# Kernel tuning notes

Measured on AMD Instinct MI355X. Metric: run time of the kernel, lower is better.

The kernel has to match this reference:

```python
import jax, jax.numpy as jnp
import numpy as np

B, N_IN, D, K, N = 8, 256, 128, 1024, 4096
EMA_GAMMA = 0.99


def setup_inputs() -> dict:
    key = jax.random.key(0)
    k1, k2, k3 = jax.random.split(key, 3)
    z = jax.random.normal(k1, (B, N_IN, N), dtype=jnp.float32)
    # Conv1d(n_in, d, 1, bias=False) == a (d, n_in) matmul; xavier-ish scale
    W_lin = jax.random.normal(k2, (D, N_IN), dtype=jnp.float32) * (1.0 / np.sqrt(N_IN))
    # codebook initialized xavier_uniform with gain=10 in the original
    lim = 10.0 * np.sqrt(6.0 / (K + D))
    emb = jax.random.uniform(k3, (K, D), dtype=jnp.float32, minval=-lim, maxval=lim)
    ema_numer = emb * (1.0 - EMA_GAMMA)
    ema_denom = jnp.ones((K,), dtype=jnp.float32) * (1.0 - EMA_GAMMA)
    return {"z": z, "W_lin": W_lin, "emb": emb,
            "ema_numer": ema_numer, "ema_denom": ema_denom}


def reference(z, W_lin, emb, ema_numer, ema_denom):
    # ze: (B, d, N) -- 1x1 conv == channel matmul
    ze = jnp.einsum('bcn,dc->bdn', z, W_lin)
    sg_emb = jax.lax.stop_gradient(emb)           # codebook is stop-gradded

    # scaled L2 distance:  ||ze - q|| / (||ze|| + ||q||), shape (B, K, N)
    ze_sq = jnp.sum(ze * ze, axis=1)              # (B, N)
    q_sq = jnp.sum(sg_emb * sg_emb, axis=1)       # (K,)
    dots = jnp.einsum('bdn,kd->bkn', ze, sg_emb)  # (B, K, N)
    dist_sq = jnp.maximum(ze_sq[:, None, :] + q_sq[None, :, None] - 2.0 * dots, 0.0)
    den = jnp.sqrt(ze_sq)[:, None, :] + jnp.sqrt(q_sq)[None, :, None]
    snorm = jnp.sqrt(dist_sq) / den               # (B, K, N)

    min_ind = jnp.argmin(snorm, axis=1)           # (B, N) int
    zq = jnp.moveaxis(sg_emb[min_ind], -1, 1)     # (B, d, N)

    # ReplaceGrad: forward value = zq, gradient routed to ze (straight-through)
    zq_rg = ze + jax.lax.stop_gradient(zq - ze)

    # EMA codebook statistics (scatter-add over codebook indices)
    flat_ind = min_ind.reshape(-1)                             # (B*N,)
    ze_flat = jax.lax.stop_gradient(
        jnp.moveaxis(ze, 1, 2).reshape(-1, ze.shape[1]))       # (B*N, d)
    z_sum = jax.ops.segment_sum(ze_flat, flat_ind, num_segments=K)   # (K, d)
    n_sum = jax.ops.segment_sum(jnp.ones(flat_ind.shape, ze.dtype),
                                flat_ind, num_segments=K)            # (K,)
    ema_numer_new = EMA_GAMMA * ema_numer + (1.0 - EMA_GAMMA) * z_sum
    ema_denom_new = EMA_GAMMA * ema_denom + (1.0 - EMA_GAMMA) * n_sum
    return zq_rg, ema_numer_new, ema_denom_new
```

## Files before the change

kernel.cpp:

```cpp
#include <hip/hip_runtime.h>
#include <cmath>
#include <stdint.h>

#define B_    8
#define NIN_  256
#define D_    128
#define K_    1024
#define N_    4096
#define P_    (B_ * N_)
#define MARGIN_M 1e-4f

typedef __attribute__((ext_vector_type(8))) short bf16x8;
typedef __attribute__((ext_vector_type(4))) float f32x4;

#define WS_ZSUM   0
#define WS_CNT    524288
#define WS_FLAGC  528384
#define WS_MEMSET 532480
#define WS_OFF    532480
#define WS_QSQ    536576
#define WS_QNORM  540672
#define WS_KSTAR  544768
#define WS_RANK   675840
#define WS_PLIST  806912
#define WS_KLIST  937984
#define WS_FLIST  1069056
#define WS_WT     1200128
#define WS_ZPM    1331200
#define WS_ZESQ   18108416
#define WS_ZEN    18239488
#define WS_ZE2F   18370560
#define WS_EMB2F  43536384
#define WS_VAL1   44322816
#define WS_IDX1   46419968
#define WS_VAL2   48517120

__device__ inline unsigned short f2bf(float v) {
  union { float f; uint32_t u; } c; c.f = v;
  return (unsigned short)((c.u + 0x7FFFu + ((c.u >> 16) & 1u)) >> 16);
}
__device__ inline float bf2f(unsigned short b) {
  union { float f; uint32_t u; } c; c.u = ((uint32_t)b) << 16; return c.f;
}
__device__ inline uint32_t pack2(float a, float b, int lo) {
  unsigned short ha = f2bf(a); if (lo) ha = f2bf(a - bf2f(ha));
  unsigned short hb = f2bf(b); if (lo) hb = f2bf(b - bf2f(hb));
  return (uint32_t)ha | ((uint32_t)hb << 16);
}

__device__ inline void gl_lds(const uint4* g, uint4* l) {
  __builtin_amdgcn_global_load_lds(
      (const __attribute__((address_space(1))) unsigned int*)g,
      (__attribute__((address_space(3))) unsigned int*)l, 16, 0, 0);
}

__global__ __launch_bounds__(256) void prep_kernel(
    const float* __restrict__ W, const float* __restrict__ emb,
    float* __restrict__ Wt, float* __restrict__ q_sq, float* __restrict__ q_norm,
    uint4* __restrict__ emb2f, uint4* __restrict__ wszero)
{
  const int tid = threadIdx.x;
  const int bid = blockIdx.x;
  if (bid < 128) {
    int t = bid * 256 + tid;
    int c = t >> 7, d = t & 127;
    Wt[t] = W[d * NIN_ + c];
  } else if (bid < 132) {
    int k = (bid - 128) * 256 + tid;
    const float* e = emb + (size_t)k * D_;
    float s = 0.f;
    #pragma unroll 8
    for (int d = 0; d < D_; ++d) s = fmaf(e[d], e[d], s);
    q_sq[k] = s;
    q_norm[k] = sqrtf(s);
  } else if (bid < 196) {
    const int kt = bid - 132;
    #pragma unroll
    for (int i = 0; i < 3; ++i) {
      int f    = i * 256 + tid;
      int c    = f >> 6;
      int lane = f & 63;
      int k    = kt * 16 + (lane & 15);
      int q    = lane >> 4;
      int kk0  = c * 32 + q * 8;
      int lo   = (kk0 >> 7) == 1;
      int d0   = kk0 & 127;
      float4 v0 = *(const float4*)&emb[(size_t)k * D_ + d0];
      float4 v1 = *(const float4*)&emb[(size_t)k * D_ + d0 + 4];
      uint4 u;
      u.x = pack2(v0.x, v0.y, lo);
      u.y = pack2(v0.z, v0.w, lo);
      u.z = pack2(v1.x, v1.y, lo);
      u.w = pack2(v1.z, v1.w, lo);
      emb2f[(size_t)kt * 768 + f] = u;
    }
  } else {
    int t = (bid - 196) * 256 + tid;
    wszero[t] = make_uint4(0u, 0u, 0u, 0u);
  }
}

__global__ __launch_bounds__(512) void ze_kernel(
    const float* __restrict__ z, const float* __restrict__ Wt,
    float* __restrict__ ze_pm, float* __restrict__ ze_sq,
    float* __restrict__ ze_norm, uint4* __restrict__ ze2f)
{
  __shared__ float tile[64][132];
  __shared__ float sqpart[8][64];
  const int t    = threadIdx.x;
  const int lane = t & 63;
  const int wv   = __builtin_amdgcn_readfirstlane(t >> 6);
  const int p    = blockIdx.x * 64 + lane;
  const int b    = p >> 12;
  const int n    = p & (N_ - 1);

  float acc[16];
  #pragma unroll
  for (int j = 0; j < 16; ++j) acc[j] = 0.f;
  const float* zp = z + (size_t)b * NIN_ * N_ + n;
  const float* wp = Wt + wv * 16;
  #pragma unroll 8
  for (int c = 0; c < NIN_; ++c) {
    float zv = zp[(size_t)c * N_];
    #pragma unroll
    for (int j = 0; j < 8; ++j)
      acc[j] = fmaf(wp[c * D_ + j], zv, acc[j]);
  }
  #pragma unroll 8
  for (int c = 0; c < NIN_; ++c) {
    float zv = zp[(size_t)c * N_];
    #pragma unroll
    for (int j = 8; j < 16; ++j)
      acc[j] = fmaf(wp[c * D_ + j], zv, acc[j]);
  }
  #pragma unroll
  for (int j = 0; j < 16; ++j) tile[lane][wv * 16 + j] = acc[j];
  float s = 0.f;
  #pragma unroll
  for (int j = 0; j < 16; ++j) s = fmaf(acc[j], acc[j], s);
  sqpart[wv][lane] = s;
  __syncthreads();
  if (wv == 0) {
    float tt = sqpart[0][lane];
    #pragma unroll
    for (int w = 1; w < 8; ++w) tt += sqpart[w][lane];
    ze_sq[p] = tt;
    ze_norm[p] = sqrtf(tt);
  }
  const int row = t >> 5;
  const int c4  = (t & 31) * 4;
  #pragma unroll
  for (int r = 0; r < 4; ++r) {
    int pr = r * 16 + row;
    float4 v = *(const float4*)&tile[pr][c4];
    *(float4*)&ze_pm[(size_t)(blockIdx.x * 64 + pr) * D_ + c4] = v;
  }
  #pragma unroll
  for (int i = 0; i < 6; ++i) {
    int f    = i * 512 + t;
    int lane_f = f & 63;
    int g    = f >> 6;
    int c    = g % 12;
    int lpt  = g / 12;
    int pl   = lpt * 16 + (lane_f & 15);
    int q    = lane_f >> 4;
    int kk0  = c * 32 + q * 8;
    int lo   = (kk0 >> 7) == 2;
    int d0   = kk0 & 127;
    float4 v0 = *(const float4*)&tile[pl][d0];
    float4 v1 = *(const float4*)&tile[pl][d0 + 4];
    uint4 u;
    u.x = pack2(v0.x, v0.y, lo);
    u.y = pack2(v0.z, v0.w, lo);
    u.z = pack2(v1.x, v1.y, lo);
    u.w = pack2(v1.z, v1.w, lo);
    ze2f[((size_t)(blockIdx.x * 4 + lpt) * 12 + c) * 64 + lane_f] = u;
  }
}

__global__ __launch_bounds__(256, 4) void mfma_argmin_kernel(
    const uint4* __restrict__ ze2f, const uint4* __restrict__ emb2f,
    const float* __restrict__ ze_sq, const float* __restrict__ ze_norm,
    const float* __restrict__ q_sq, const float* __restrict__ q_norm,
    float* __restrict__ val1, int* __restrict__ idx1, float* __restrict__ val2)
{
  __shared__ uint4 Ls[2][16][64];
  const int tid  = threadIdx.x;
  const int lane = tid & 63;
  const int w    = __builtin_amdgcn_readfirstlane(tid >> 6);
  const int x    = blockIdx.x & 7;
  const int ib   = blockIdx.x >> 3;
  const int pb3  = x * 32 + (ib & 31);
  const int kb2  = ib >> 5;
  const int pt0  = pb3 * 8;
  const int ct0  = kb2 * 8;
  const int wm   = w >> 1;
  const int wn   = w & 1;
  const int wq   = w * 4;
  const int wm4  = wm * 4;
  const int wn4  = wn * 4;

  const uint4* sbase = (w < 2)
      ? ze2f  + ((size_t)(pt0 + w * 4) * 12) * 64 + lane
      : emb2f + ((size_t)(ct0 + (w - 2) * 4) * 12) * 64 + lane;

  f32x4 acc[4][4];
  #pragma unroll
  for (int ii = 0; ii < 4; ++ii)
    #pragma unroll
    for (int jj = 0; jj < 4; ++jj) acc[ii][jj] = (f32x4){0.f, 0.f, 0.f, 0.f};

#define STAGE(NB, C)                                                        \
  gl_lds(sbase + 0 * 768 + (C) * 64, &Ls[NB][wq + 0][0]);                   \
  gl_lds(sbase + 1 * 768 + (C) * 64, &Ls[NB][wq + 1][0]);                   \
  gl_lds(sbase + 2 * 768 + (C) * 64, &Ls[NB][wq + 2][0]);                   \
  gl_lds(sbase + 3 * 768 + (C) * 64, &Ls[NB][wq + 3][0]);

#define MFMA_STEP(CUR)                                                      \
  {                                                                         \
    uint4 afr[4], bfr[4];                                                   \
    afr[0] = Ls[CUR][wm4 + 0][lane];  afr[1] = Ls[CUR][wm4 + 1][lane];      \
    afr[2] = Ls[CUR][wm4 + 2][lane];  afr[3] = Ls[CUR][wm4 + 3][lane];      \
    bfr[0] = Ls[CUR][8 + wn4 + 0][lane]; bfr[1] = Ls[CUR][8 + wn4 + 1][lane]; \
    bfr[2] = Ls[CUR][8 + wn4 + 2][lane]; bfr[3] = Ls[CUR][8 + wn4 + 3][lane]; \
    __builtin_amdgcn_s_setprio(1);                                          \
    _Pragma("unroll")                                                       \
    for (int ii = 0; ii < 4; ++ii) {                                        \
      union { uint4 u; bf16x8 h; } au; au.u = afr[ii];                      \
      _Pragma("unroll")                                                     \
      for (int jj = 0; jj < 4; ++jj) {                                      \
        union { uint4 u; bf16x8 h; } bu; bu.u = bfr[jj];                    \
        acc[ii][jj] = __builtin_amdgcn_mfma_f32_16x16x32_bf16(au.h, bu.h,   \
                                                        acc[ii][jj], 0, 0, 0); \
      }                                                                     \
    }                                                                       \
    __builtin_amdgcn_s_setprio(0);                                          \
  }

#define STEP_MID(C, CUR, NXT)                                               \
  STAGE(NXT, (C) + 1)                                                       \
  asm volatile("s_waitcnt vmcnt(4)" ::: "memory");                          \
  __builtin_amdgcn_s_barrier();                                             \
  __builtin_amdgcn_sched_barrier(0);                                        \
  MFMA_STEP(CUR)                                                            \
  __builtin_amdgcn_s_barrier();                                             \
  __builtin_amdgcn_sched_barrier(0);

  STAGE(0, 0)
  STEP_MID(0, 0, 1)  STEP_MID(1, 1, 0)  STEP_MID(2, 0, 1)  STEP_MID(3, 1, 0)
  STEP_MID(4, 0, 1)  STEP_MID(5, 1, 0)  STEP_MID(6, 0, 1)  STEP_MID(7, 1, 0)
  STEP_MID(8, 0, 1)  STEP_MID(9, 1, 0)  STEP_MID(10, 0, 1)
  asm volatile("s_waitcnt vmcnt(0)" ::: "memory");
  __builtin_amdgcn_s_barrier();
  __builtin_amdgcn_sched_barrier(0);
  MFMA_STEP(1)

#undef STEP_MID
#undef MFMA_STEP
#undef STAGE

  const int col = lane & 15;
  const int q   = lane >> 4;
  float qsq_l[4], qn_l[4]; int kg[4];
  #pragma unroll
  for (int j = 0; j < 4; ++j) {
    kg[j]    = kb2 * 128 + wn * 64 + j * 16 + col;
    qsq_l[j] = q_sq[kg[j]];
    qn_l[j]  = q_norm[kg[j]];
  }
  const int g = kb2 * 2 + wn;
  #pragma unroll
  for (int ii = 0; ii < 4; ++ii) {
    const int pbase = pb3 * 128 + wm * 64 + ii * 16 + q * 4;
    f32x4 zs = *(const f32x4*)&ze_sq[pbase];
    f32x4 zn = *(const f32x4*)&ze_norm[pbase];
    float m1r[4], m2r[4]; int k1r[4];
    #pragma unroll
    for (int r = 0; r < 4; ++r) { m1r[r] = 1e30f; m2r[r] = 1e30f; k1r[r] = 0; }
    #pragma unroll
    for (int j = 0; j < 4; ++j) {
      #pragma unroll
      for (int r = 0; r < 4; ++r) {
        float dsq = fmaxf(zs[r] + qsq_l[j] - 2.0f * acc[ii][j][r], 0.0f);
        float den = zn[r] + qn_l[j];
        float rd  = __builtin_amdgcn_rcpf(den);
        float m   = dsq * rd * rd;
        bool take = m < m1r[r];
        float loser = take ? m1r[r] : m;
        if (take) { m1r[r] = m; k1r[r] = kg[j]; }
        m2r[r] = fminf(m2r[r], loser);
      }
    }
    #pragma unroll
    for (int ms = 1; ms <= 8; ms <<= 1) {
      #pragma unroll
      for (int r = 0; r < 4; ++r) {
        float om1 = __shfl_xor(m1r[r], ms);
        int   ok1 = __shfl_xor(k1r[r], ms);
        float om2 = __shfl_xor(m2r[r], ms);
        bool take = (om1 < m1r[r]) || (om1 == m1r[r] && ok1 < k1r[r]);
        float loser = take ? m1r[r] : om1;
        if (take) { m1r[r] = om1; k1r[r] = ok1; }
        m2r[r] = fminf(fminf(m2r[r], om2), loser);
      }
    }
    if (col == 0) {
      const size_t o = (size_t)g * P_ + pbase;
      *(float4*)&val1[o] = make_float4(m1r[0], m1r[1], m1r[2], m1r[3]);
      *(int4*)&idx1[o]   = make_int4(k1r[0], k1r[1], k1r[2], k1r[3]);
      *(float4*)&val2[o] = make_float4(m2r[0], m2r[1], m2r[2], m2r[3]);
    }
  }
}

__global__ __launch_bounds__(256) void resolve_kernel(
    const float* __restrict__ val1, const int* __restrict__ idx1,
    const float* __restrict__ val2, int* __restrict__ kstar,
    int* __restrict__ rank, int* __restrict__ counts,
    int* __restrict__ flaglist, int* __restrict__ flagcnt)
{
  const int p = blockIdx.x * 256 + threadIdx.x;
  float m1 = 1e30f, m2 = 1e30f; int k1 = 0;
  #pragma unroll
  for (int g = 0; g < 16; ++g) {
    float v1 = val1[(size_t)g * P_ + p];
    int   i1 = idx1[(size_t)g * P_ + p];
    float v2 = val2[(size_t)g * P_ + p];
    bool take = v1 < m1;
    float loser = take ? m1 : v1;
    if (take) { m1 = v1; k1 = i1; }
    m2 = fminf(fminf(m2, v2), loser);
  }
  kstar[p] = k1;
  if (m2 - m1 <= MARGIN_M) {
    int s = atomicAdd(flagcnt, 1);
    flaglist[s] = p;
  } else {
    rank[p] = atomicAdd(&counts[k1], 1);
  }
}

__global__ __launch_bounds__(256) void fallback_kernel(
    const float* __restrict__ ze_pm, const float* __restrict__ emb,
    const float* __restrict__ ze_sq, const float* __restrict__ ze_norm,
    const float* __restrict__ q_sq, const float* __restrict__ q_norm,
    const int* __restrict__ flaglist, const int* __restrict__ flagcnt,
    int* __restrict__ kstar, int* __restrict__ rank, int* __restrict__ counts)
{
  __shared__ float zlds[128];
  __shared__ float wbs[4];
  __shared__ int   wbk[4];
  const int tid  = threadIdx.x;
  const int lane = tid & 63;
  const int w    = tid >> 6;
  const int cnt  = *flagcnt;
  for (int i = blockIdx.x; i < cnt; i += gridDim.x) {
    const int p = flaglist[i];
    __syncthreads();
    if (tid < 128) zlds[tid] = ze_pm[(size_t)p * D_ + tid];
    __syncthreads();
    const float zsq = ze_sq[p], zn = ze_norm[p];
    float bs = 1e30f; int bk = 0;
    #pragma unroll
    for (int tt = 0; tt < 4; ++tt) {
      const int k = (w * 4 + tt) * 64 + lane;
      const float* e = emb + (size_t)k * D_;
      float dot = 0.f;
      #pragma unroll 8
      for (int d = 0; d < D_; ++d)
        dot = fmaf(zlds[d], e[d], dot);
      float dsq = fmaxf(fmaf(-2.0f, dot, zsq + q_sq[k]), 0.0f);
      float sn  = sqrtf(dsq) / (zn + q_norm[k]);
      if (sn < bs) { bs = sn; bk = k; }
    }
    #pragma unroll
    for (int m = 1; m <= 32; m <<= 1) {
      float ov = __shfl_xor(bs, m);
      int   ok = __shfl_xor(bk, m);
      if (ov < bs || (ov == bs && ok < bk)) { bs = ov; bk = ok; }
    }
    if (lane == 0) { wbs[w] = bs; wbk[w] = bk; }
    __syncthreads();
    if (tid == 0) {
      float fb = wbs[0]; int fk = wbk[0];
      #pragma unroll
      for (int ww = 1; ww < 4; ++ww) {
        if (wbs[ww] < fb) { fb = wbs[ww]; fk = wbk[ww]; }
      }
      kstar[p] = fk;
      rank[p] = atomicAdd(&counts[fk], 1);
    }
  }
}

__global__ __launch_bounds__(1024) void prefix_kernel(
    const int* __restrict__ counts, const float* __restrict__ ema_denom,
    int* __restrict__ offsets, float* __restrict__ out_den)
{
  __shared__ int s[1024];
  const int t = threadIdx.x;
  const int c = counts[t];
  s[t] = c;
  __syncthreads();
  for (int off = 1; off < 1024; off <<= 1) {
    int v = (t >= off) ? s[t - off] : 0;
    __syncthreads();
    s[t] += v;
    __syncthreads();
  }
  offsets[t] = s[t] - c;
  out_den[t] = 0.99f * ema_denom[t] + 0.01f * (float)c;
}

__global__ __launch_bounds__(256) void scatter_kernel(
    const int* __restrict__ kstar, const int* __restrict__ rank,
    const int* __restrict__ offsets, int* __restrict__ pos_list,
    int* __restrict__ k_list)
{
  const int p = blockIdx.x * 256 + threadIdx.x;
  const int k = kstar[p];
  const int slot = offsets[k] + rank[p];
  pos_list[slot] = p;
  k_list[slot] = k;
}

__global__ __launch_bounds__(512) void zq_kernel(
    const float* __restrict__ ze_pm, const float* __restrict__ emb,
    const int* __restrict__ kstar, float* __restrict__ out)
{
  const int tid = threadIdx.x;
  const int lane = tid & 63;
  const int w = __builtin_amdgcn_readfirstlane(tid >> 6);
  const int p = blockIdx.x * 64 + lane;
  const int b = p >> 12;
  const int n = p & (N_ - 1);
  const int kst = kstar[p];
  const float* zr = ze_pm + (size_t)p * D_ + w * 16;
  const float* ek = emb + (size_t)kst * D_ + w * 16;
  float* op = out + (size_t)b * D_ * N_ + (size_t)(w * 16) * N_ + n;
  float4 zv[4], ev[4];
  #pragma unroll
  for (int r = 0; r < 4; ++r) {
    zv[r] = *(const float4*)&zr[r * 4];
    ev[r] = *(const float4*)&ek[r * 4];
  }
  #pragma unroll
  for (int r = 0; r < 4; ++r) {
    const float* zc = (const float*)&zv[r];
    const float* ec = (const float*)&ev[r];
    #pragma unroll
    for (int jj = 0; jj < 4; ++jj) {
      float zev = zc[jj];
      op[(size_t)(r * 4 + jj) * N_] = zev + (ec[jj] - zev);
    }
  }
}

__global__ __launch_bounds__(128) void gsum_kernel(
    const float* __restrict__ ze_pm, const int* __restrict__ pos_list,
    const int* __restrict__ k_list, float* __restrict__ z_sum)
{
  const int d  = threadIdx.x;
  const int i0 = blockIdx.x * 32;
  int   kprev = -1;
  float acc = 0.f;
  #pragma unroll
  for (int ii = 0; ii < 32; ++ii) {
    int p = pos_list[i0 + ii];
    int k = k_list[i0 + ii];
    if (k != kprev) {
      if (kprev >= 0) atomicAdd(&z_sum[(size_t)kprev * D_ + d], acc);
      acc = 0.f;
      kprev = k;
    }
    acc += ze_pm[(size_t)p * D_ + d];
  }
  if (kprev >= 0) atomicAdd(&z_sum[(size_t)kprev * D_ + d], acc);
}

__global__ __launch_bounds__(256) void finalize_num_kernel(
    const float* __restrict__ ema_numer, const float* __restrict__ z_sum,
    float* __restrict__ out)
{
  const int t = blockIdx.x * 256 + threadIdx.x;
  float* out_num = out + (size_t)B_ * D_ * N_;
  out_num[t] = 0.99f * ema_numer[t] + 0.01f * z_sum[t];
}

extern "C" void kernel_launch(void* const* d_in, const int* in_sizes, int n_in,
                              void* d_out, int out_size, void* d_ws, size_t ws_size,
                              hipStream_t stream)
{
  (void)in_sizes; (void)n_in; (void)out_size; (void)ws_size;
  const float* z         = (const float*)d_in[0];
  const float* W         = (const float*)d_in[1];
  const float* emb       = (const float*)d_in[2];
  const float* ema_numer = (const float*)d_in[3];
  const float* ema_denom = (const float*)d_in[4];
  float* out = (float*)d_out;
  char*  ws  = (char*)d_ws;
  float* z_sum   = (float*)(ws + WS_ZSUM);
  int*   counts  = (int*)(ws + WS_CNT);
  int*   flagcnt = (int*)(ws + WS_FLAGC);
  int*   offsets = (int*)(ws + WS_OFF);
  float* q_sq    = (float*)(ws + WS_QSQ);
  float* q_norm  = (float*)(ws + WS_QNORM);
  int*   kstar   = (int*)(ws + WS_KSTAR);
  int*   rank    = (int*)(ws + WS_RANK);
  int*   plist   = (int*)(ws + WS_PLIST);
  int*   klist   = (int*)(ws + WS_KLIST);
  int*   flist   = (int*)(ws + WS_FLIST);
  float* Wt      = (float*)(ws + WS_WT);
  float* ze_pm   = (float*)(ws + WS_ZPM);
  float* ze_sq   = (float*)(ws + WS_ZESQ);
  float* ze_norm = (float*)(ws + WS_ZEN);
  uint4* ze2f    = (uint4*)(ws + WS_ZE2F);
  uint4* emb2f   = (uint4*)(ws + WS_EMB2F);
  float* val1    = (float*)(ws + WS_VAL1);
  int*   idx1    = (int*)(ws + WS_IDX1);
  float* val2    = (float*)(ws + WS_VAL2);
  float* out_den = out + (size_t)B_ * D_ * N_ + K_ * D_;

  prep_kernel<<<326, 256, 0, stream>>>(W, emb, Wt, q_sq, q_norm, emb2f,
                                       (uint4*)ws);
  ze_kernel<<<P_ / 64, 512, 0, stream>>>(z, Wt, ze_pm, ze_sq, ze_norm, ze2f);
  mfma_argmin_kernel<<<2048, 256, 0, stream>>>(ze2f, emb2f, ze_sq, ze_norm,
                                               q_sq, q_norm, val1, idx1, val2);
  resolve_kernel<<<P_ / 256, 256, 0, stream>>>(val1, idx1, val2, kstar,
                                               rank, counts, flist, flagcnt);
  fallback_kernel<<<1024, 256, 0, stream>>>(ze_pm, emb, ze_sq, ze_norm,
                                            q_sq, q_norm, flist, flagcnt,
                                            kstar, rank, counts);
  prefix_kernel<<<1, 1024, 0, stream>>>(counts, ema_denom, offsets, out_den);
  scatter_kernel<<<P_ / 256, 256, 0, stream>>>(kstar, rank, offsets, plist, klist);
  zq_kernel<<<P_ / 64, 512, 0, stream>>>(ze_pm, emb, kstar, out);
  gsum_kernel<<<P_ / 32, 128, 0, stream>>>(ze_pm, plist, klist, z_sum);
  finalize_num_kernel<<<K_ * D_ / 256, 256, 0, stream>>>(ema_numer, z_sum, out);
}
```

Baseline: 245.4 us.

## Fuse scatter into zq kernel and add dim-major ze copy for coalesced reads

The separate scatter kernel is folded into zq_kernel, with wave 0 writing pos_list/k_list, which removes one launch. ze_kernel can also write a dim-major copy of ze (d by position) when the workspace is large enough. zq_kernel then reads ze with coalesced per-dimension loads instead of strided point-major float4 loads. The cost is an extra 16 MB write in ze_kernel and a dependence on workspace size, falling back to the old path otherwise.

```diff
diff --git a/kernel.cpp b/kernel.cpp
--- a/kernel.cpp
+++ b/kernel.cpp
@@ -34,6 +34,8 @@
 #define WS_VAL1   44322816
 #define WS_IDX1   46419968
 #define WS_VAL2   48517120
+#define WS_ZDM    50614272
+#define WS_END    (WS_ZDM + P_ * D_ * 4)
 
 __device__ inline unsigned short f2bf(float v) {
   union { float f; uint32_t u; } c; c.f = v;
@@ -103,7 +105,8 @@
 __global__ __launch_bounds__(512) void ze_kernel(
     const float* __restrict__ z, const float* __restrict__ Wt,
     float* __restrict__ ze_pm, float* __restrict__ ze_sq,
-    float* __restrict__ ze_norm, uint4* __restrict__ ze2f)
+    float* __restrict__ ze_norm, uint4* __restrict__ ze2f,
+    float* __restrict__ ze_dm)
 {
   __shared__ float tile[64][132];
   __shared__ float sqpart[8][64];
@@ -132,6 +135,11 @@
     #pragma unroll
     for (int j = 8; j < 16; ++j)
       acc[j] = fmaf(wp[c * D_ + j], zv, acc[j]);
+  }
+  if (ze_dm) {
+    #pragma unroll
+    for (int j = 0; j < 16; ++j)
+      ze_dm[(size_t)(wv * 16 + j) * P_ + p] = acc[j];
   }
   #pragma unroll
   for (int j = 0; j < 16; ++j) tile[lane][wv * 16 + j] = acc[j];
@@ -412,21 +420,12 @@
   out_den[t] = 0.99f * ema_denom[t] + 0.01f * (float)c;
 }
 
-__global__ __launch_bounds__(256) void scatter_kernel(
-    const int* __restrict__ kstar, const int* __restrict__ rank,
-    const int* __restrict__ offsets, int* __restrict__ pos_list,
-    int* __restrict__ k_list)
-{
-  const int p = blockIdx.x * 256 + threadIdx.x;
-  const int k = kstar[p];
-  const int slot = offsets[k] + rank[p];
-  pos_list[slot] = p;
-  k_list[slot] = k;
-}
-
 __global__ __launch_bounds__(512) void zq_kernel(
-    const float* __restrict__ ze_pm, const float* __restrict__ emb,
-    const int* __restrict__ kstar, float* __restrict__ out)
+    const float* __restrict__ ze_pm, const float* __restrict__ ze_dm,
+    const float* __restrict__ emb, const int* __restrict__ kstar,
+    const int* __restrict__ rank, const int* __restrict__ offsets,
+    int* __restrict__ pos_list, int* __restrict__ k_list,
+    float* __restrict__ out)
 {
   const int tid = threadIdx.x;
   const int lane = tid & 63;
@@ -435,23 +434,47 @@
   const int b = p >> 12;
   const int n = p & (N_ - 1);
   const int kst = kstar[p];
-  const float* zr = ze_pm + (size_t)p * D_ + w * 16;
+
+  if (w == 0) {
+    const int slot = offsets[kst] + rank[p];
+    pos_list[slot] = p;
+    k_list[slot] = kst;
+  }
+
   const float* ek = emb + (size_t)kst * D_ + w * 16;
   float* op = out + (size_t)b * D_ * N_ + (size_t)(w * 16) * N_ + n;
-  float4 zv[4], ev[4];
-  #pragma unroll
-  for (int r = 0; r < 4; ++r) {
-    zv[r] = *(const float4*)&zr[r * 4];
-    ev[r] = *(const float4*)&ek[r * 4];
-  }
-  #pragma unroll
-  for (int r = 0; r < 4; ++r) {
-    const float* zc = (const float*)&zv[r];
-    const float* ec = (const float*)&ev[r];
-    #pragma unroll
-    for (int jj = 0; jj < 4; ++jj) {
-      float zev = zc[jj];
-      op[(size_t)(r * 4 + jj) * N_] = zev + (ec[jj] - zev);
+  float4 ev[4];
+  #pragma unroll
+  for (int r = 0; r < 4; ++r) ev[r] = *(const float4*)&ek[r * 4];
+
+  if (ze_dm) {
+    float zv[16];
+    #pragma unroll
+    for (int j = 0; j < 16; ++j)
+      zv[j] = ze_dm[(size_t)(w * 16 + j) * P_ + p];
+    #pragma unroll
+    for (int r = 0; r < 4; ++r) {
+      const float* ec = (const float*)&ev[r];
+      #pragma unroll
+      for (int jj = 0; jj < 4; ++jj) {
+        float zev = zv[r * 4 + jj];
+        op[(size_t)(r * 4 + jj) * N_] = zev + (ec[jj] - zev);
+      }
+    }
+  } else {
+    const float* zr = ze_pm + (size_t)p * D_ + w * 16;
+    float4 zv[4];
+    #pragma unroll
+    for (int r = 0; r < 4; ++r) zv[r] = *(const float4*)&zr[r * 4];
+    #pragma unroll
+    for (int r = 0; r < 4; ++r) {
+      const float* zc = (const float*)&zv[r];
+      const float* ec = (const float*)&ev[r];
+      #pragma unroll
+      for (int jj = 0; jj < 4; ++jj) {
+        float zev = zc[jj];
+        op[(size_t)(r * 4 + jj) * N_] = zev + (ec[jj] - zev);
+      }
     }
   }
 }
@@ -491,7 +514,7 @@
                               void* d_out, int out_size, void* d_ws, size_t ws_size,
                               hipStream_t stream)
 {
-  (void)in_sizes; (void)n_in; (void)out_size; (void)ws_size;
+  (void)in_sizes; (void)n_in; (void)out_size;
   const float* z         = (const float*)d_in[0];
   const float* W         = (const float*)d_in[1];
   const float* emb       = (const float*)d_in[2];
@@ -519,11 +542,14 @@
   float* val1    = (float*)(ws + WS_VAL1);
   int*   idx1    = (int*)(ws + WS_IDX1);
   float* val2    = (float*)(ws + WS_VAL2);
+  float* ze_dm   = (ws_size >= (size_t)WS_END) ? (float*)(ws + WS_ZDM)
+                                               : (float*)nullptr;
   float* out_den = out + (size_t)B_ * D_ * N_ + K_ * D_;
 
   prep_kernel<<<326, 256, 0, stream>>>(W, emb, Wt, q_sq, q_norm, emb2f,
                                        (uint4*)ws);
-  ze_kernel<<<P_ / 64, 512, 0, stream>>>(z, Wt, ze_pm, ze_sq, ze_norm, ze2f);
+  ze_kernel<<<P_ / 64, 512, 0, stream>>>(z, Wt, ze_pm, ze_sq, ze_norm, ze2f,
+                                         ze_dm);
   mfma_argmin_kernel<<<2048, 256, 0, stream>>>(ze2f, emb2f, ze_sq, ze_norm,
                                                q_sq, q_norm, val1, idx1, val2);
   resolve_kernel<<<P_ / 256, 256, 0, stream>>>(val1, idx1, val2, kstar,
@@ -532,8 +558,8 @@
                                             q_sq, q_norm, flist, flagcnt,
                                             kstar, rank, counts);
   prefix_kernel<<<1, 1024, 0, stream>>>(counts, ema_denom, offsets, out_den);
-  scatter_kernel<<<P_ / 256, 256, 0, stream>>>(kstar, rank, offsets, plist, klist);
-  zq_kernel<<<P_ / 64, 512, 0, stream>>>(ze_pm, emb, kstar, out);
+  zq_kernel<<<P_ / 64, 512, 0, stream>>>(ze_pm, ze_dm, emb, kstar, rank,
+                                         offsets, plist, klist, out);
   gsum_kernel<<<P_ / 32, 128, 0, stream>>>(ze_pm, plist, klist, z_sum);
   finalize_num_kernel<<<K_ * D_ / 256, 256, 0, stream>>>(ema_numer, z_sum, out);
 }
```

New measurement: 248.8 us. No clear change (+1.4%).
